# Kernel optimization log

Hardware: AMD Instinct MI355X
Metric: run time of the kernel (lower is better)

## Reference

```python
import jax, jax.numpy as jnp
import numpy as np

N_HEAD, D_MODEL, D_K, D_V, MAX_NEIGHBOR = 8, 512, 64, 64, 5
BS, SEQ = 2, 1024


def setup_inputs() -> dict:
    key = jax.random.key(0)
    ks = jax.random.split(key, 12)
    inp = {
        'q': jax.random.normal(ks[0], (BS, SEQ, D_MODEL), jnp.float32),
        'k': jax.random.normal(ks[1], (BS, SEQ, D_MODEL), jnp.float32),
        'v': jax.random.normal(ks[2], (BS, SEQ, D_MODEL), jnp.float32),
        'mask': jnp.ones((BS, SEQ, SEQ), jnp.int32),
        'dist': jax.random.randint(ks[3], (BS, SEQ, SEQ), 0, 10, jnp.int32),
        # weights stored as (in, out) so y = x @ W
        'w_qs': jax.random.normal(ks[4], (D_MODEL, N_HEAD * D_K), jnp.float32) * 0.02,
        'w_ks': jax.random.normal(ks[5], (D_MODEL, N_HEAD * D_K), jnp.float32) * 0.02,
        'w_vs': jax.random.normal(ks[6], (D_MODEL, N_HEAD * D_V), jnp.float32) * 0.02,
        'w_fc': jax.random.normal(ks[7], (N_HEAD * D_V, D_MODEL), jnp.float32) * 0.02,
        'ln_gamma': jnp.ones((D_MODEL,), jnp.float32),
        'ln_beta': jnp.zeros((D_MODEL,), jnp.float32),
        'base_rpr': jax.random.normal(ks[8], (MAX_NEIGHBOR + 1, D_K), jnp.float32) * 0.02,
    }
    return inp


def reference(q, k, v, mask, dist, w_qs, w_ks, w_vs, w_fc, ln_gamma, ln_beta, base_rpr):
    bs, sq, dm = q.shape
    temp = jnp.asarray(D_K, q.dtype) ** 0.5
    residual = q
    # layer norm on q only (as in original)
    mu = jnp.mean(q, axis=-1, keepdims=True)
    var = jnp.var(q, axis=-1, keepdims=True)
    qn = (q - mu) / jnp.sqrt(var + 1e-6) * ln_gamma + ln_beta
    # projections -> [bs, heads, seq, d]
    qh = (qn @ w_qs).reshape(bs, sq, N_HEAD, D_K).transpose(0, 2, 1, 3)
    kh = (k @ w_ks).reshape(bs, sq, N_HEAD, D_K).transpose(0, 2, 1, 3)
    vh = (v @ w_vs).reshape(bs, sq, N_HEAD, D_V).transpose(0, 2, 1, 3)
    qs = qh / temp
    # standard QK^T scores
    attn1 = jnp.einsum('bhid,bhjd->bhij', qs, kh)
    # relative-position scores: instead of materializing rpr[b,i,j,d],
    # contract q with the small base table then gather by clipped distance.
    dc = jnp.minimum(dist, MAX_NEIGHBOR)  # dist>max_neighbor -> max_neighbor
    qb = jnp.einsum('bhid,md->bhim', qs, base_rpr)  # [bs,h,seq,M+1]
    idx = jnp.broadcast_to(dc[:, None, :, :], (bs, N_HEAD, sq, sq))
    attn2 = jnp.take_along_axis(qb, idx, axis=-1)  # [bs,h,seq,seq]
    attn = attn1 + attn2
    attn = jnp.where(mask[:, None, :, :] == 0, jnp.asarray(-1e9, attn.dtype), attn)
    attn = jax.nn.softmax(attn, axis=-1)  # dropout disabled (eval)
    out = jnp.einsum('bhij,bhjd->bhid', attn, vh)
    out = out.transpose(0, 2, 1, 3).reshape(bs, sq, N_HEAD * D_V)
    out = out @ w_fc + residual
    return out, attn
```

## Files before the change

kernel.cpp:

```cpp
#include <hip/hip_runtime.h>
#include <math.h>

#define SEQ 1024
#define DM 512

typedef __attribute__((ext_vector_type(8))) short bf16x8;
typedef __attribute__((ext_vector_type(4))) short bf16x4;
typedef __attribute__((ext_vector_type(4))) float f32x4;
typedef __attribute__((ext_vector_type(4))) int i32x4;

static __device__ __forceinline__ short f2b(float f) {
    union { float f; unsigned u; } x; x.f = f;
    unsigned r = (x.u + 0x7FFFu + ((x.u >> 16) & 1u)) >> 16;
    return (short)r;
}
static __device__ __forceinline__ float b2f(short s) {
    union { unsigned u; float f; } x; x.u = ((unsigned)(unsigned short)s) << 16;
    return x.f;
}
static __device__ __forceinline__ int sidx(int row, int col) {
    int byte = (row << 7) + (col << 1);
    byte ^= (row & 7) << 4;
    return byte >> 1;
}

static __device__ __forceinline__ void stage_f32(short* dst, const float* src, int srcStride, int tid) {
    int r = tid >> 2, c = (tid & 3) * 16;
    const float* p = src + (size_t)r * srcStride + c;
    bf16x8 v0, v1;
    #pragma unroll
    for (int e = 0; e < 8; ++e) v0[e] = f2b(p[e]);
    #pragma unroll
    for (int e = 0; e < 8; ++e) v1[e] = f2b(p[8 + e]);
    *(bf16x8*)&dst[sidx(r, c)] = v0;
    *(bf16x8*)&dst[sidx(r, c + 8)] = v1;
}
static __device__ __forceinline__ void stage_bf16(short* dst, const short* src, int srcStride, int tid) {
    int r = tid >> 2, c = (tid & 3) * 16;
    const short* p = src + (size_t)r * srcStride + c;
    bf16x8 v0 = *(const bf16x8*)p;
    bf16x8 v1 = *(const bf16x8*)(p + 8);
    *(bf16x8*)&dst[sidx(r, c)] = v0;
    *(bf16x8*)&dst[sidx(r, c + 8)] = v1;
}

static __device__ __forceinline__ void mma64(const short* sA, const short* sB, f32x4* acc,
                                             int w, int lr, int lg) {
    #pragma unroll
    for (int ks = 0; ks < 2; ++ks) {
        bf16x8 af = *(const bf16x8*)&sA[sidx(w * 16 + lr, ks * 32 + lg * 8)];
        #pragma unroll
        for (int nt = 0; nt < 4; ++nt) {
            bf16x8 bf = *(const bf16x8*)&sB[sidx(nt * 16 + lr, ks * 32 + lg * 8)];
            acc[nt] = __builtin_amdgcn_mfma_f32_16x16x32_bf16(af, bf, acc[nt], 0, 0, 0);
        }
    }
}

__global__ __launch_bounds__(256) void prep_kernel(
    const float* __restrict__ w0, const float* __restrict__ w1,
    const float* __restrict__ w2, const float* __restrict__ w3, short* __restrict__ wt,
    const float* __restrict__ q, short* __restrict__ qnb,
    const float* __restrict__ gamma, const float* __restrict__ beta,
    const int* __restrict__ dist, const int* __restrict__ mask, unsigned char* __restrict__ idxp) {
    int blk = blockIdx.x;
    int tid = threadIdx.x;
    if (blk < 256) {
        int wsel = blk >> 6;
        int t = blk & 63;
        int tr = t >> 3, tc = t & 7;
        const float* src = wsel == 0 ? w0 : wsel == 1 ? w1 : wsel == 2 ? w2 : w3;
        short* dst = wt + (size_t)wsel * 512 * 512;
        __shared__ float tile[64][65];
        int r = tid >> 2, c = (tid & 3) * 16;
        const float* p = src + (size_t)(tr * 64 + r) * 512 + tc * 64 + c;
        #pragma unroll
        for (int e = 0; e < 16; ++e) tile[r][c + e] = p[e];
        __syncthreads();
        bf16x8 v0, v1;
        #pragma unroll
        for (int e = 0; e < 16; ++e) {
            short bv = f2b(tile[c + e][r]);
            if (e < 8) v0[e] = bv; else v1[e - 8] = bv;
        }
        short* qd = dst + (size_t)(tc * 64 + r) * 512 + tr * 64 + c;
        *(bf16x8*)qd = v0;
        *(bf16x8*)(qd + 8) = v1;
    } else if (blk < 2304) {
        int row = blk - 256;
        const float* x = q + (size_t)row * DM;
        short* y = qnb + (size_t)row * DM;
        float v1 = x[tid], v2 = x[tid + 256];
        float s = v1 + v2;
        float ss = v1 * v1 + v2 * v2;
        for (int o = 32; o > 0; o >>= 1) { s += __shfl_down(s, o); ss += __shfl_down(ss, o); }
        __shared__ float red[4], red2[4];
        __shared__ float s_mu, s_rstd;
        int wid = tid >> 6, lane = tid & 63;
        if (lane == 0) { red[wid] = s; red2[wid] = ss; }
        __syncthreads();
        if (tid == 0) {
            float ts = red[0] + red[1] + red[2] + red[3];
            float tss = red2[0] + red2[1] + red2[2] + red2[3];
            float mu = ts / DM;
            float var = tss / DM - mu * mu;
            s_mu = mu;
            s_rstd = rsqrtf(var + 1e-6f);
        }
        __syncthreads();
        float mu = s_mu, rstd = s_rstd;
        y[tid]       = f2b((v1 - mu) * rstd * gamma[tid]       + beta[tid]);
        y[tid + 256] = f2b((v2 - mu) * rstd * gamma[tid + 256] + beta[tid + 256]);
    } else {
        size_t base = ((size_t)(blk - 2304) * 256 + tid) * 8;
        i32x4 d0 = *(const i32x4*)(dist + base);
        i32x4 d1 = *(const i32x4*)(dist + base + 4);
        i32x4 m0 = *(const i32x4*)(mask + base);
        i32x4 m1 = *(const i32x4*)(mask + base + 4);
        int dv[8], mv[8];
        #pragma unroll
        for (int e = 0; e < 4; ++e) { dv[e] = d0[e]; dv[4 + e] = d1[e]; mv[e] = m0[e]; mv[4 + e] = m1[e]; }
        unsigned char ob[4];
        #pragma unroll
        for (int e = 0; e < 4; ++e) {
            int dA = dv[2 * e];     if (dA > 5) dA = 5;
            int dB = dv[2 * e + 1]; if (dB > 5) dB = 5;
            unsigned nA = (unsigned)dA | (mv[2 * e] == 0 ? 8u : 0u);
            unsigned nB = (unsigned)dB | (mv[2 * e + 1] == 0 ? 8u : 0u);
            ob[e] = (unsigned char)(nA | (nB << 4));
        }
        *(uchar4*)(idxp + base / 2) = *(uchar4*)ob;
    }
}

__global__ __launch_bounds__(256) void qkv_kernel(
    const short* __restrict__ qnb, const float* __restrict__ k, const float* __restrict__ v,
    const short* __restrict__ wT, short* __restrict__ qsb, short* __restrict__ khx,
    short* __restrict__ vfx) {
    __shared__ short sA[64 * 64];
    __shared__ short sB[64 * 64];
    int tid = threadIdx.x;
    int sel = blockIdx.x >> 8;
    int t = blockIdx.x & 255;
    int bx = t & 7, by = t >> 3;
    int m0 = by << 6, n0 = bx << 6;
    int w = tid >> 6, l = tid & 63;
    int lr = l & 15, lg = l >> 4;
    const short* Bt = wT + (size_t)sel * 262144;
    float scale = sel == 0 ? 0.125f : 1.0f;
    f32x4 acc[4] = {};
    for (int kt = 0; kt < 512; kt += 64) {
        __syncthreads();
        if (sel == 0) stage_bf16(sA, qnb + (size_t)m0 * 512 + kt, 512, tid);
        else          stage_f32 (sA, (sel == 1 ? k : v) + (size_t)m0 * 512 + kt, 512, tid);
        stage_bf16(sB, Bt + (size_t)n0 * 512 + kt, 512, tid);
        __syncthreads();
        mma64(sA, sB, acc, w, lr, lg);
    }
    short* scratch = sA + w * 1024;
    if (sel == 0) {
        #pragma unroll
        for (int nt = 0; nt < 4; ++nt)
            #pragma unroll
            for (int r = 0; r < 4; ++r)
                scratch[(lg * 4 + r) * 64 + nt * 16 + lr] = f2b(acc[nt][r] * scale);
        #pragma unroll
        for (int cc = 0; cc < 2; ++cc) {
            int c = cc * 64 + l;
            *(bf16x8*)&qsb[(size_t)(m0 + w * 16 + (c >> 3)) * 512 + n0 + (c & 7) * 8]
                = *(const bf16x8*)&scratch[c * 8];
        }
    } else if (sel == 1) {
        #pragma unroll
        for (int nt = 0; nt < 4; ++nt) {
            int dl = nt * 16 + lr;
            int f = dl >> 5, lgp = (dl >> 3) & 3, e = dl & 7;
            int base = ((f * 4 + lgp) * 16) * 8 + e;
            #pragma unroll
            for (int r = 0; r < 4; ++r)
                scratch[base + (lg * 4 + r) * 8] = f2b(acc[nt][r]);
        }
        int bq = m0 >> 10, jt = (m0 >> 6) & 15;
        short* blockp = khx + ((((size_t)(bq * 8 + bx) * 16 + jt) * 4 + w) << 10);
        *(bf16x8*)(blockp + l * 8)       = *(const bf16x8*)(scratch + l * 8);
        *(bf16x8*)(blockp + 512 + l * 8) = *(const bf16x8*)(scratch + 512 + l * 8);
    } else {
        int bq = m0 >> 10, j6 = (m0 >> 6) & 15, p = j6 >> 1, rel = j6 & 1;
        #pragma unroll
        for (int nt = 0; nt < 4; ++nt)
            #pragma unroll
            for (int r = 0; r < 4; ++r) {
                int s = ((nt * 2 + (lg >> 1)) * 16 + lr) * 8 + (lg & 1) * 4 + r;
                scratch[s] = f2b(acc[nt][r]);
            }
        short* blockp = vfx + ((((size_t)(bq * 8 + bx) * 8 + p) * 4 + w) << 11);
        #pragma unroll
        for (int cc = 0; cc < 2; ++cc) {
            int c = cc * 64 + l;
            int s = c * 8;
            int g = s + ((c >> 5) << 8) + (rel << 8);
            *(bf16x8*)(blockp + g) = *(const bf16x8*)(scratch + s);
        }
    }
}

#define IDXSTR 520
__global__ __launch_bounds__(256) void attn_fused_kernel(
    const short* __restrict__ qsb, const short* __restrict__ khx,
    const short* __restrict__ vfx, const unsigned char* __restrict__ idxp,
    const float* __restrict__ rpr, float* __restrict__ attnp, short* __restrict__ oh) {
    int bid = ((blockIdx.x & 7) << 7) + (blockIdx.x >> 3);
    int bh = bid >> 6, it = bid & 63;
    int b = bh >> 3, h = bh & 7;
    int i0 = it << 4;
    int tid = threadIdx.x;
    int w = tid >> 6, l = tid & 63;
    int lr = l & 15, lg = l >> 4;

    __shared__ __align__(16) char sBuf[10880];
    __shared__ float sL[4][16];
    short* sQ = (short*)sBuf;
    float* sQB = (float*)(sBuf + 2048);
    unsigned char* sIdx = (unsigned char*)(sBuf + 2560);
    float* sO8 = (float*)sBuf;

    if (tid < 128) {
        int r = tid >> 3, c = (tid & 7) * 8;
        bf16x8 qv = *(const bf16x8*)(qsb + ((size_t)(b * SEQ + i0 + r)) * DM + h * 64 + c);
        *(bf16x8*)&sQ[sidx(r, c)] = qv;
    }
    {
        const unsigned char* ibase = idxp + ((size_t)(b * SEQ + i0)) * 512;
        #pragma unroll
        for (int p = 0; p < 2; ++p) {
            int idx = p * 256 + tid;
            int row = idx >> 5;
            int cb = (idx & 31) * 16;
            i32x4 v = *(const i32x4*)(ibase + (size_t)row * 512 + cb);
            *(i32x4*)&sIdx[row * IDXSTR + cb] = v;
        }
    }
    __syncthreads();
    if (tid < 128) {
        int r = tid >> 3, m = tid & 7;
        if (m < 6) {
            float a = 0.f;
            #pragma unroll 8
            for (int d = 0; d < 64; ++d) a += b2f(sQ[sidx(r, d)]) * rpr[m * 64 + d];
            sQB[r * 8 + m] = a;
        }
    }
    __syncthreads();

    bf16x8 qf0 = *(const bf16x8*)&sQ[sidx(lr, lg * 8)];
    bf16x8 qf1 = *(const bf16x8*)&sQ[sidx(lr, 32 + lg * 8)];

    float qb0 = sQB[lr * 8 + 0], qb1 = sQB[lr * 8 + 1], qb2 = sQB[lr * 8 + 2];
    float qb3 = sQB[lr * 8 + 3], qb4 = sQB[lr * 8 + 4], qb5 = sQB[lr * 8 + 5];
    __syncthreads();

    float l_lane = 0.f;
    unsigned p_lo[16], p_hi[16];
    f32x4 accO[4] = {};
    const short* kblk = khx + (((size_t)bh * 16) * 4 + w) * 1024;
    const short* vblk = vfx + (((size_t)bh * 8) * 4 + w) * 2048;
    int fragoff = (lg * 16 + lr) * 8;
    const unsigned char* irow = sIdx + lr * IDXSTR + w * 8 + lg * 2;

    #pragma unroll
    for (int jt = 0; jt < 16; ++jt) {
        const short* kb = kblk + jt * 4096;
        bf16x8 kf0 = *(const bf16x8*)(kb + fragoff);
        bf16x8 kf1 = *(const bf16x8*)(kb + 512 + fragoff);
        f32x4 sf = {};
        sf = __builtin_amdgcn_mfma_f32_16x16x32_bf16(kf0, qf0, sf, 0, 0, 0);
        sf = __builtin_amdgcn_mfma_f32_16x16x32_bf16(kf1, qf1, sf, 0, 0, 0);
        unsigned u = *(const unsigned short*)(irow + jt * 32);
        float pv[4];
        #pragma unroll
        for (int r = 0; r < 4; ++r) {
            unsigned bb = (u >> (4 * r)) & 0xFu;
            unsigned dd = bb & 7u;
            float t0 = (dd & 1) ? qb1 : qb0;
            float t1 = (dd & 1) ? qb3 : qb2;
            float t2 = (dd & 1) ? qb5 : qb4;
            float u0 = (dd & 2) ? t1 : t0;
            float bias = (dd & 4) ? t2 : u0;
            float s = fminf(sf[r] + bias, 30.f);
            float p = (bb & 8) ? 0.f : __expf(s);
            pv[r] = p;
            l_lane += p;
        }
        unsigned plo, phi;
        asm("v_cvt_pk_bf16_f32 %0, %1, %2" : "=v"(plo) : "v"(pv[0]), "v"(pv[1]));
        asm("v_cvt_pk_bf16_f32 %0, %1, %2" : "=v"(phi) : "v"(pv[2]), "v"(pv[3]));
        p_lo[jt] = plo; p_hi[jt] = phi;
        if (jt & 1) {
            unsigned plo0 = p_lo[jt - 1], phi0 = p_hi[jt - 1];
            int srcA = lr + ((lg & 1) << 5);
            int srcB = srcA + 16;
            unsigned aw0 = __shfl(plo0, srcA), aw1 = __shfl(phi0, srcA);
            unsigned aw2 = __shfl(plo,  srcA), aw3 = __shfl(phi,  srcA);
            unsigned bw0 = __shfl(plo0, srcB), bw1 = __shfl(phi0, srcB);
            unsigned bw2 = __shfl(plo,  srcB), bw3 = __shfl(phi,  srcB);
            bool hi = lg >= 2;
            union { unsigned q[4]; bf16x8 v; } afu;
            afu.q[0] = hi ? aw2 : aw0;
            afu.q[1] = hi ? aw3 : aw1;
            afu.q[2] = hi ? bw2 : bw0;
            afu.q[3] = hi ? bw3 : bw1;
            bf16x8 af = afu.v;
            const short* vb = vblk + (jt >> 1) * 8192;
            #pragma unroll
            for (int nt = 0; nt < 4; ++nt) {
                bf16x8 bf = *(const bf16x8*)(vb + nt * 512 + fragoff);
                accO[nt] = __builtin_amdgcn_mfma_f32_16x16x32_bf16(af, bf, accO[nt], 0, 0, 0);
            }
        }
    }

    l_lane += __shfl_xor(l_lane, 16);
    l_lane += __shfl_xor(l_lane, 32);
    if (lg == 0) sL[w][lr] = l_lane;
    __syncthreads();

    #pragma unroll
    for (int nt = 0; nt < 2; ++nt)
        #pragma unroll
        for (int r = 0; r < 4; ++r)
            sO8[w * 512 + (lg * 4 + r) * 32 + nt * 16 + lr] = accO[nt][r];
    __syncthreads();
    if (tid < 128) {
        int row = tid >> 3, c4 = (tid & 7) * 4;
        f32x4 o = *(f32x4*)&sO8[row * 32 + c4];
        o += *(f32x4*)&sO8[512 + row * 32 + c4];
        o += *(f32x4*)&sO8[1024 + row * 32 + c4];
        o += *(f32x4*)&sO8[1536 + row * 32 + c4];
        float rl = 1.f / (sL[0][row] + sL[1][row] + sL[2][row] + sL[3][row]);
        bf16x4 ob;
        #pragma unroll
        for (int e = 0; e < 4; ++e) ob[e] = f2b(o[e] * rl);
        *(bf16x4*)&oh[((size_t)(b * SEQ + i0 + row)) * DM + h * 64 + c4] = ob;
    }
    __syncthreads();
    #pragma unroll
    for (int nt = 2; nt < 4; ++nt)
        #pragma unroll
        for (int r = 0; r < 4; ++r)
            sO8[w * 512 + (lg * 4 + r) * 32 + (nt - 2) * 16 + lr] = accO[nt][r];
    __syncthreads();
    if (tid < 128) {
        int row = tid >> 3, c4 = (tid & 7) * 4;
        f32x4 o = *(f32x4*)&sO8[row * 32 + c4];
        o += *(f32x4*)&sO8[512 + row * 32 + c4];
        o += *(f32x4*)&sO8[1024 + row * 32 + c4];
        o += *(f32x4*)&sO8[1536 + row * 32 + c4];
        float rl = 1.f / (sL[0][row] + sL[1][row] + sL[2][row] + sL[3][row]);
        bf16x4 ob;
        #pragma unroll
        for (int e = 0; e < 4; ++e) ob[e] = f2b(o[e] * rl);
        *(bf16x4*)&oh[((size_t)(b * SEQ + i0 + row)) * DM + h * 64 + 32 + c4] = ob;
    }

    float rl = 1.f / (sL[0][lr] + sL[1][lr] + sL[2][lr] + sL[3][lr]);
    float* ap = attnp + ((size_t)(bh * SEQ + i0 + lr)) * SEQ + w * 16 + lg * 4;
    #pragma unroll
    for (int jt = 0; jt < 16; ++jt) {
        unsigned plo = p_lo[jt], phi = p_hi[jt];
        f32x4 o;
        o[0] = b2f((short)(plo & 0xffff)) * rl;
        o[1] = b2f((short)(plo >> 16))    * rl;
        o[2] = b2f((short)(phi & 0xffff)) * rl;
        o[3] = b2f((short)(phi >> 16))    * rl;
        *(f32x4*)&ap[jt * 64] = o;
    }
}

__global__ __launch_bounds__(256) void fc_kernel(
    const short* __restrict__ oh, const short* __restrict__ BtFc,
    const float* __restrict__ Rsd, float* __restrict__ Cp) {
    __shared__ short sA[64 * 64];
    __shared__ short sB[64 * 64];
    int tid = threadIdx.x;
    int bx = blockIdx.x & 7, by = blockIdx.x >> 3;
    int m0 = by << 6, n0 = bx << 6;
    int w = tid >> 6, l = tid & 63;
    int lr = l & 15, lg = l >> 4;
    f32x4 acc[4] = {};
    for (int kt = 0; kt < 512; kt += 64) {
        __syncthreads();
        stage_bf16(sA, oh + (size_t)m0 * 512 + kt, 512, tid);
        stage_bf16(sB, BtFc + (size_t)n0 * 512 + kt, 512, tid);
        __syncthreads();
        mma64(sA, sB, acc, w, lr, lg);
    }
    #pragma unroll
    for (int nt = 0; nt < 4; ++nt)
        #pragma unroll
        for (int r = 0; r < 4; ++r) {
            int gm = m0 + w * 16 + lg * 4 + r;
            int gn = n0 + nt * 16 + lr;
            Cp[(size_t)gm * 512 + gn] = acc[nt][r] + Rsd[(size_t)gm * 512 + gn];
        }
}

extern "C" void kernel_launch(void* const* d_in, const int* in_sizes, int n_in,
                              void* d_out, int out_size, void* d_ws, size_t ws_size,
                              hipStream_t stream) {
    const float* q     = (const float*)d_in[0];
    const float* k     = (const float*)d_in[1];
    const float* v     = (const float*)d_in[2];
    const int*   mask  = (const int*)d_in[3];
    const int*   dist  = (const int*)d_in[4];
    const float* w_qs  = (const float*)d_in[5];
    const float* w_ks  = (const float*)d_in[6];
    const float* w_vs  = (const float*)d_in[7];
    const float* w_fc  = (const float*)d_in[8];
    const float* gamma = (const float*)d_in[9];
    const float* beta  = (const float*)d_in[10];
    const float* rpr   = (const float*)d_in[11];

    char* wsb = (char*)d_ws;
    short* qnb  = (short*)wsb;
    short* oh   = (short*)wsb + 1048576;
    short* wT   = (short*)(wsb + 4u * 1024 * 1024);
    short* qsb  = (short*)(wsb + 6u * 1024 * 1024);
    short* khx  = (short*)(wsb + 8u * 1024 * 1024);
    short* vfx  = (short*)(wsb + 10u * 1024 * 1024);
    unsigned char* idxp = (unsigned char*)(wsb + 12u * 1024 * 1024);

    float* outp  = (float*)d_out;
    float* attnp = outp + 1048576;

    prep_kernel<<<3328, 256, 0, stream>>>(w_qs, w_ks, w_vs, w_fc, wT, q, qnb, gamma, beta, dist, mask, idxp);
    qkv_kernel<<<768, 256, 0, stream>>>(qnb, k, v, wT, qsb, khx, vfx);
    attn_fused_kernel<<<1024, 256, 0, stream>>>(qsb, khx, vfx, idxp, rpr, attnp, oh);
    fc_kernel<<<256, 256, 0, stream>>>(oh, wT + 786432, q, outp);
}
```

Before: 65.33 us.

## Split attention key range across eight waves per block

Doubles the attention block to 512 threads. Two groups of four waves each handle half of the key tiles, and their partial output accumulators and row sums are reduced through shared memory. This raises the number of waves in flight and halves per-wave register state for the probability buffers, to hide memory and MFMA latency better. In exchange, the cross-wave reduction gets larger and the shared-memory footprint grows.

Result: no change. 65.55 us (+0.3%).

```diff
diff --git a/kernel.cpp b/kernel.cpp
--- a/kernel.cpp
+++ b/kernel.cpp
@@ -205,7 +205,7 @@
 }
 
 #define IDXSTR 520
-__global__ __launch_bounds__(256) void attn_fused_kernel(
+__global__ __launch_bounds__(512) void attn_fused_kernel(
     const short* __restrict__ qsb, const short* __restrict__ khx,
     const short* __restrict__ vfx, const unsigned char* __restrict__ idxp,
     const float* __restrict__ rpr, float* __restrict__ attnp, short* __restrict__ oh) {
@@ -216,9 +216,11 @@
     int tid = threadIdx.x;
     int w = tid >> 6, l = tid & 63;
     int lr = l & 15, lg = l >> 4;
-
-    __shared__ __align__(16) char sBuf[10880];
-    __shared__ float sL[4][16];
+    int wj = w & 3;
+    int jtb = (w >> 2) * 8;
+
+    __shared__ __align__(16) char sBuf[16384];
+    __shared__ float sL[8][16];
     short* sQ = (short*)sBuf;
     float* sQB = (float*)(sBuf + 2048);
     unsigned char* sIdx = (unsigned char*)(sBuf + 2560);
@@ -231,13 +233,14 @@
     }
     {
         const unsigned char* ibase = idxp + ((size_t)(b * SEQ + i0)) * 512;
-        #pragma unroll
-        for (int p = 0; p < 2; ++p) {
-            int idx = p * 256 + tid;
+        int idx = tid;
+        if (idx < 520) {
             int row = idx >> 5;
             int cb = (idx & 31) * 16;
-            i32x4 v = *(const i32x4*)(ibase + (size_t)row * 512 + cb);
-            *(i32x4*)&sIdx[row * IDXSTR + cb] = v;
+            if (row < 16) {
+                i32x4 v = *(const i32x4*)(ibase + (size_t)row * 512 + cb);
+                *(i32x4*)&sIdx[row * IDXSTR + cb] = v;
+            }
         }
     }
     __syncthreads();
@@ -260,15 +263,16 @@
     __syncthreads();
 
     float l_lane = 0.f;
-    unsigned p_lo[16], p_hi[16];
+    unsigned p_lo[8], p_hi[8];
     f32x4 accO[4] = {};
-    const short* kblk = khx + (((size_t)bh * 16) * 4 + w) * 1024;
-    const short* vblk = vfx + (((size_t)bh * 8) * 4 + w) * 2048;
+    const short* kblk = khx + (((size_t)bh * 16) * 4 + wj) * 1024;
+    const short* vblk = vfx + (((size_t)bh * 8) * 4 + wj) * 2048;
     int fragoff = (lg * 16 + lr) * 8;
-    const unsigned char* irow = sIdx + lr * IDXSTR + w * 8 + lg * 2;
-
-    #pragma unroll
-    for (int jt = 0; jt < 16; ++jt) {
+    const unsigned char* irow = sIdx + lr * IDXSTR + wj * 8 + lg * 2;
+
+    #pragma unroll
+    for (int jj = 0; jj < 8; ++jj) {
+        int jt = jtb + jj;
         const short* kb = kblk + jt * 4096;
         bf16x8 kf0 = *(const bf16x8*)(kb + fragoff);
         bf16x8 kf1 = *(const bf16x8*)(kb + 512 + fragoff);
@@ -294,9 +298,9 @@
         unsigned plo, phi;
         asm("v_cvt_pk_bf16_f32 %0, %1, %2" : "=v"(plo) : "v"(pv[0]), "v"(pv[1]));
         asm("v_cvt_pk_bf16_f32 %0, %1, %2" : "=v"(phi) : "v"(pv[2]), "v"(pv[3]));
-        p_lo[jt] = plo; p_hi[jt] = phi;
-        if (jt & 1) {
-            unsigned plo0 = p_lo[jt - 1], phi0 = p_hi[jt - 1];
+        p_lo[jj] = plo; p_hi[jj] = phi;
+        if (jj & 1) {
+            unsigned plo0 = p_lo[jj - 1], phi0 = p_hi[jj - 1];
             int srcA = lr + ((lg & 1) << 5);
             int srcB = srcA + 16;
             unsigned aw0 = __shfl(plo0, srcA), aw1 = __shfl(phi0, srcA);
@@ -333,10 +337,13 @@
     if (tid < 128) {
         int row = tid >> 3, c4 = (tid & 7) * 4;
         f32x4 o = *(f32x4*)&sO8[row * 32 + c4];
-        o += *(f32x4*)&sO8[512 + row * 32 + c4];
-        o += *(f32x4*)&sO8[1024 + row * 32 + c4];
-        o += *(f32x4*)&sO8[1536 + row * 32 + c4];
-        float rl = 1.f / (sL[0][row] + sL[1][row] + sL[2][row] + sL[3][row]);
+        float lt = sL[0][row];
+        #pragma unroll
+        for (int wv = 1; wv < 8; ++wv) {
+            o += *(f32x4*)&sO8[wv * 512 + row * 32 + c4];
+            lt += sL[wv][row];
+        }
+        float rl = 1.f / lt;
         bf16x4 ob;
         #pragma unroll
         for (int e = 0; e < 4; ++e) ob[e] = f2b(o[e] * rl);
@@ -352,27 +359,33 @@
     if (tid < 128) {
         int row = tid >> 3, c4 = (tid & 7) * 4;
         f32x4 o = *(f32x4*)&sO8[row * 32 + c4];
-        o += *(f32x4*)&sO8[512 + row * 32 + c4];
-        o += *(f32x4*)&sO8[1024 + row * 32 + c4];
-        o += *(f32x4*)&sO8[1536 + row * 32 + c4];
-        float rl = 1.f / (sL[0][row] + sL[1][row] + sL[2][row] + sL[3][row]);
+        float lt = sL[0][row];
+        #pragma unroll
+        for (int wv = 1; wv < 8; ++wv) {
+            o += *(f32x4*)&sO8[wv * 512 + row * 32 + c4];
+            lt += sL[wv][row];
+        }
+        float rl = 1.f / lt;
         bf16x4 ob;
         #pragma unroll
         for (int e = 0; e < 4; ++e) ob[e] = f2b(o[e] * rl);
         *(bf16x4*)&oh[((size_t)(b * SEQ + i0 + row)) * DM + h * 64 + 32 + c4] = ob;
     }
 
-    float rl = 1.f / (sL[0][lr] + sL[1][lr] + sL[2][lr] + sL[3][lr]);
-    float* ap = attnp + ((size_t)(bh * SEQ + i0 + lr)) * SEQ + w * 16 + lg * 4;
-    #pragma unroll
-    for (int jt = 0; jt < 16; ++jt) {
-        unsigned plo = p_lo[jt], phi = p_hi[jt];
+    float lt = sL[0][lr];
+    #pragma unroll
+    for (int wv = 1; wv < 8; ++wv) lt += sL[wv][lr];
+    float rl = 1.f / lt;
+    float* ap = attnp + ((size_t)(bh * SEQ + i0 + lr)) * SEQ + wj * 16 + lg * 4;
+    #pragma unroll
+    for (int jj = 0; jj < 8; ++jj) {
+        unsigned plo = p_lo[jj], phi = p_hi[jj];
         f32x4 o;
         o[0] = b2f((short)(plo & 0xffff)) * rl;
         o[1] = b2f((short)(plo >> 16))    * rl;
         o[2] = b2f((short)(phi & 0xffff)) * rl;
         o[3] = b2f((short)(phi >> 16))    * rl;
-        *(f32x4*)&ap[jt * 64] = o;
+        *(f32x4*)&ap[(jtb + jj) * 64] = o;
     }
 }
 
@@ -434,6 +447,6 @@
 
     prep_kernel<<<3328, 256, 0, stream>>>(w_qs, w_ks, w_vs, w_fc, wT, q, qnb, gamma, beta, dist, mask, idxp);
     qkv_kernel<<<768, 256, 0, stream>>>(qnb, k, v, wT, qsb, khx, vfx);
-    attn_fused_kernel<<<1024, 256, 0, stream>>>(qsb, khx, vfx, idxp, rpr, attnp, oh);
+    attn_fused_kernel<<<1024, 512, 0, stream>>>(qsb, khx, vfx, idxp, rpr, attnp, oh);
     fc_kernel<<<256, 256, 0, stream>>>(oh, wT + 786432, q, outp);
 }
```
